# Optimization experiments

Hardware: AMD Instinct MI355X
Metric: run time of the kernel (lower is better)

## Reference

```python
import jax, jax.numpy as jnp
import numpy as np

# CUBA-LIF constants (from LavaNetwork.__init__ with beta=0.95)
THRESHOLD = 1.0
CURRENT_DECAY = 1.0   # current[t] = (1-1.0)*current[t-1] + input[t] == input[t]
VOLTAGE_DECAY = 1.0 - 0.95  # = 0.05, so v[t] = 0.95*v[t-1] + cur[t]

N_INPUT, N_HIDDEN, N_OUTPUT = 512, 2048, 4 * 64
B, T = 32, 1024


def setup_inputs() -> dict:
    key = jax.random.key(0)
    kx, k1, k2, k3, k4 = jax.random.split(key, 5)
    x = (jax.random.uniform(kx, (B, N_INPUT, T)) < 0.1).astype(jnp.float32)
    # learned params (Linear with bias); small scale so spiking is reasonable
    w1 = jax.random.normal(k1, (N_HIDDEN, N_INPUT), dtype=jnp.float32) * (1.0 / np.sqrt(N_INPUT))
    b1 = jax.random.normal(k2, (N_HIDDEN,), dtype=jnp.float32) * 0.01
    w2 = jax.random.normal(k3, (N_OUTPUT, N_HIDDEN), dtype=jnp.float32) * (1.0 / np.sqrt(N_HIDDEN))
    b2 = jax.random.normal(k4, (N_OUTPUT,), dtype=jnp.float32) * 0.01
    return {"x": x, "w1": w1, "b1": b1, "w2": w2, "b2": b2}


def _cuba_lif(cur):
    """CUBA neuron with current_decay=1 (current==synaptic input),
    leaky-integrate voltage, fire at threshold, reset voltage to 0.
    cur: (B, N, T) -> spikes (B, N, T)."""
    beta_v = 1.0 - VOLTAGE_DECAY  # 0.95

    def step(v, c_t):
        v = v * beta_v + c_t
        s = (v >= THRESHOLD).astype(v.dtype)
        v = v * (1.0 - s)  # reset-to-zero on spike (Loihi behavior)
        return v, s

    cur_t = jnp.moveaxis(cur, -1, 0)  # (T, B, N)
    v0 = jnp.zeros(cur.shape[:-1], cur.dtype)
    _, spk = jax.lax.scan(step, v0, cur_t)
    return jnp.moveaxis(spk, 0, -1)  # (B, N, T)


def reference(x, w1, b1, w2, b2):
    # layer 1: synapse (einsum 'bit,oi->bot' + bias) -> CUBA neuron
    cur1 = jnp.einsum('bit,oi->bot', x, w1) + b1[None, :, None]
    spk1 = _cuba_lif(cur1)
    # layer 2
    cur2 = jnp.einsum('bit,oi->bot', spk1, w2) + b2[None, :, None]
    spk2 = _cuba_lif(cur2)
    return (spk1, spk2)
```

## Files before the change

### kernel.cpp

```cpp
#include <hip/hip_runtime.h>


typedef int i32x4 __attribute__((ext_vector_type(4)));
typedef _Float16 f16x8 __attribute__((ext_vector_type(8)));
typedef _Float16 f16x4 __attribute__((ext_vector_type(4)));
typedef float f32x4 __attribute__((ext_vector_type(4)));

#define GLDS(g, l) __builtin_amdgcn_global_load_lds( \
    (const __attribute__((address_space(1))) void*)(g), \
    (__attribute__((address_space(3))) void*)(l), 16, 0, 0)

#define INV231 4.656612873077392578125e-10


__global__ __launch_bounds__(256) void prep_w8(const float* __restrict__ A,
                                               signed char* __restrict__ wp,
                                               int M, int K)
{
    long gt = (long)blockIdx.x * 256 + threadIdx.x;
    int kq4 = K >> 2;
    int m = (int)(gt / kq4), kq = (int)(gt % kq4);
    int k0 = kq * 4;
    int kt = k0 >> 6, kin = k0 & 63;
    int cw = ((kin >> 4) ^ (m >> 1)) & 3;
    float4 w = *(const float4*)&A[(long)m * K + k0];
    float wv[4] = {w.x, w.y, w.z, w.w};
    int pack[4] = {0, 0, 0, 0};
#pragma unroll
    for (int e = 0; e < 4; e++) {
        long k64 = (long)rint((double)wv[e] * 2147483648.0);
#pragma unroll
        for (int j = 0; j < 3; j++) {
            long r = ((k64 + 128) & 255) - 128;
            pack[j] |= ((int)r & 255) << (e * 8);
            k64 = (k64 - r) >> 8;
        }
        pack[3] |= ((int)k64 & 255) << (e * 8);
    }
#pragma unroll
    for (int p = 0; p < 4; p++)
        *(int*)&wp[(((long)kt * 4 + p) * M + m) * 64 + cw * 16 + (kin & 15)] = pack[p];
}

__global__ __launch_bounds__(256) void prep_x8(const float* __restrict__ x,
                                               unsigned char* __restrict__ xt)
{
    __shared__ float xs[64][68];
    const int b = blockIdx.z, i0 = blockIdx.y * 64, t0 = blockIdx.x * 64;
    const float* xb = x + ((long)b * 512 + i0) * 1024 + t0;
#pragma unroll
    for (int p = 0; p < 4; p++) {
        int f = threadIdx.x + p * 256;
        int i = f >> 4, t4 = (f & 15) * 4;
        *(float4*)&xs[i][t4] = *(const float4*)&xb[(long)i * 1024 + t4];
    }
    __syncthreads();
    int tt = threadIdx.x >> 2, c = threadIdx.x & 3;
    unsigned char bytes[16];
#pragma unroll
    for (int j = 0; j < 16; j++)
        bytes[j] = (unsigned char)xs[c * 16 + j][tt];
    *(uint4*)&xt[(((long)b * 8 + (i0 >> 6)) * 1024 + t0 + tt) * 64 + c * 16] =
        *(uint4*)bytes;
}

__global__ __launch_bounds__(320, 1) void gemm_lif1(
    const signed char* __restrict__ wp,
    const unsigned char* __restrict__ act,
    const float* __restrict__ bias,
    unsigned* __restrict__ mask_ws)
{
    __shared__ signed char Ws[8][4][64][64];
    __shared__ float cs[2][64][64];

    const int m0 = blockIdx.x * 64, b = blockIdx.y;
    const int tid = threadIdx.x, lane = tid & 63, wave = tid >> 6;
    const int lm = lane & 15, lq = lane >> 4;
    const int fro = ((lq ^ (lm >> 1)) & 3) * 16;
    const unsigned char* ab = act + (long)b * 8 * 1024 * 64;

    i32x4 areg[4][4];
    double bv = 0.0;

    if (wave < 4) {
        const int gl_row = lane >> 2, gl_col = (lane & 3) * 16;
#pragma unroll
        for (int j = 0; j < 8; ++j) {
            const int r = wave + 4 * j;
            const int kt = r >> 2, pl = r & 3;
            const signed char* g = wp + ((long)r * 2048 + m0 + gl_row) * 64 + gl_col;
#pragma unroll
            for (int q = 0; q < 4; ++q)
                GLDS(g + q * 16 * 64, &Ws[kt][pl][q * 16][0]);
        }
        bv = (double)bias[m0 + wave * 16 + lm];
#pragma unroll
        for (int f = 0; f < 4; f++)
            areg[0][f] = *(const i32x4*)
                &ab[((long)(f * 16 + lm)) * 64 + lq * 16];
#pragma unroll
        for (int f = 0; f < 4; f++)
            areg[1][f] = *(const i32x4*)
                &ab[((long)1 * 1024 + f * 16 + lm) * 64 + lq * 16];
    }
    __syncthreads();

    double u = 0.0;
    bool sprev = false;

    for (int p = 0; p < 17; ++p) {
        if (wave < 4 && p < 16) {
            i32x4 acc[4][4];
#pragma unroll
            for (int pp = 0; pp < 4; pp++)
#pragma unroll
                for (int f = 0; f < 4; f++) acc[pp][f] = (i32x4)0;

#pragma unroll
            for (int kk = 0; kk < 8; ++kk) {
                {
                    int vn = p * 8 + kk + 2;
                    if (vn > 127) vn = 127;
                    const int pn = vn >> 3, kn = vn & 7;
                    const long tt = (long)pn * 64 + lm;
#pragma unroll
                    for (int f = 0; f < 4; f++)
                        areg[(kk + 2) & 3][f] = *(const i32x4*)
                            &ab[((long)kn * 1024 + tt + f * 16) * 64 + lq * 16];
                }
                __builtin_amdgcn_s_setprio(1);
#pragma unroll
                for (int pl = 0; pl < 4; pl++) {
                    i32x4 w0 = *(const i32x4*)&Ws[kk][pl][wave * 16 + lm][fro];
#pragma unroll
                    for (int f = 0; f < 4; f++)
                        acc[pl][f] = __builtin_amdgcn_mfma_i32_16x16x64_i8(
                            areg[kk & 3][f], w0, acc[pl][f], 0, 0, 0);
                }
                __builtin_amdgcn_s_setprio(0);
            }
#pragma unroll
            for (int tf = 0; tf < 4; tf++)
#pragma unroll
                for (int r = 0; r < 4; r++) {
                    long T = acc[3][tf][r];
                    T = T * 256 + acc[2][tf][r];
                    T = T * 256 + acc[1][tf][r];
                    T = T * 256 + acc[0][tf][r];
                    cs[p & 1][tf * 16 + lq * 4 + r][wave * 16 + lm] =
                        (float)((double)T * INV231 + bv);
                }
        }
        if (wave == 4 && p >= 1) {
            const int pq = p - 1, buf = pq & 1;
            float cvA[32], cvB[32];
#pragma unroll
            for (int j = 0; j < 32; ++j) cvA[j] = cs[buf][j][lane];
#pragma unroll
            for (int j = 0; j < 32; ++j) cvB[j] = cs[buf][32 + j][lane];
            {
                unsigned mword = 0;
#pragma unroll
                for (int j = 0; j < 32; ++j) {
                    double c = (double)cvA[j];
                    double a = 0.95 * u + c;
                    u = sprev ? c : a;
                    bool s = (u >= 1.0);
                    mword |= (s ? 1u : 0u) << j;
                    sprev = s;
                }
                mask_ws[((long)b * 32 + pq * 2 + 0) * 2048 + m0 + lane] = mword;
            }
            {
                unsigned mword = 0;
#pragma unroll
                for (int j = 0; j < 32; ++j) {
                    double c = (double)cvB[j];
                    double a = 0.95 * u + c;
                    u = sprev ? c : a;
                    bool s = (u >= 1.0);
                    mword |= (s ? 1u : 0u) << j;
                    sprev = s;
                }
                mask_ws[((long)b * 32 + pq * 2 + 1) * 2048 + m0 + lane] = mword;
            }
        }
        asm volatile("s_waitcnt lgkmcnt(0)" ::: "memory");
        __builtin_amdgcn_s_barrier();
        __builtin_amdgcn_sched_barrier(0);
    }
}


__global__ __launch_bounds__(256) void expand_spk8(
    const unsigned* __restrict__ mask_ws,
    unsigned char* __restrict__ spk8)
{
    __shared__ unsigned msk[64][33];
    const int b = blockIdx.x, kt = blockIdx.y;
    const int tid = threadIdx.x;
#pragma unroll
    for (int i = 0; i < 8; ++i) {
        int idx = tid + i * 256;
        int tw = idx >> 6, m = idx & 63;
        msk[m][tw] = mask_ws[((long)b * 32 + tw) * 2048 + kt * 64 + m];
    }
    __syncthreads();
    unsigned char* dst = spk8 + ((long)b * 32 + kt) * 1024 * 64;
#pragma unroll
    for (int i = 0; i < 16; ++i) {
        int off = tid + i * 256;
        int t = off >> 2, mq = off & 3;
        int tw = t >> 5, sh = t & 31;
        unsigned w0 = 0, w1 = 0, w2 = 0, w3 = 0;
#pragma unroll
        for (int j = 0; j < 4; ++j) {
            w0 |= ((msk[mq * 16 + j][tw] >> sh) & 1u) << (8 * j);
            w1 |= ((msk[mq * 16 + 4 + j][tw] >> sh) & 1u) << (8 * j);
            w2 |= ((msk[mq * 16 + 8 + j][tw] >> sh) & 1u) << (8 * j);
            w3 |= ((msk[mq * 16 + 12 + j][tw] >> sh) & 1u) << (8 * j);
        }
        *(uint4*)&dst[(long)off * 16] = (uint4){w0, w1, w2, w3};
    }
}

__global__ __launch_bounds__(256) void expand_spk(
    const unsigned* __restrict__ mask_ws,
    float* __restrict__ spk1)
{
    __shared__ unsigned msk[8][32];
    const long rowbase = (long)blockIdx.x * 8;
    const int b = (int)(rowbase >> 11), m0 = (int)(rowbase & 2047);
    const int tid = threadIdx.x;
    {
        int w = tid >> 3, r = tid & 7;
        msk[r][w] = mask_ws[((long)b * 32 + w) * 2048 + m0 + r];
    }
    __syncthreads();
    const int r = tid >> 5, l5 = tid & 31;
    float* dst = spk1 + (rowbase + r) * 1024;
    const int sh = (l5 & 7) * 4;
#pragma unroll
    for (int j = 0; j < 8; j++) {
        const int t = l5 * 4 + j * 128;
        const unsigned w = msk[r][(l5 >> 3) + j * 4];
        float4 o;
        o.x = ((w >> sh) & 1u) ? 1.f : 0.f;
        o.y = ((w >> (sh + 1)) & 1u) ? 1.f : 0.f;
        o.z = ((w >> (sh + 2)) & 1u) ? 1.f : 0.f;
        o.w = ((w >> (sh + 3)) & 1u) ? 1.f : 0.f;
        *(float4*)&dst[t] = o;
    }
}

template <bool TRANS, int NITER, int CHUNK>
__global__ __launch_bounds__(256, 2) void gemm_i8(
    const signed char* __restrict__ wp,
    const unsigned char* __restrict__ act,
    const float* __restrict__ bias,
    float* __restrict__ C,
    int M)
{
    constexpr int NCHUNK = NITER / CHUNK;
    __shared__ signed char Ws[CHUNK][4][32][64];

    const int b = blockIdx.y;
    const int m0 = blockIdx.z * 32, t0 = blockIdx.x * 256;
    const int tid = threadIdx.x, lane = tid & 63, wave = tid >> 6;
    const int wt = t0 + wave * 64;
    const int lm = lane & 15, lq = lane >> 4;
    const int fro = ((lq ^ (lm >> 1)) & 3) * 16;
    const int gl_row = lane >> 2, gl_col = (lane & 3) * 16;

    const unsigned char* ab = act + (long)b * NITER * 1024 * 64;

    auto stage = [&](int cc) {
#pragma unroll
        for (int j = 0; j < CHUNK; ++j) {
            const int r = wave + 4 * j;
            const int kt = r >> 2, p = r & 3;
            const long kg = ((long)(cc * CHUNK + kt) * 4 + p);
            const signed char* g = wp + (kg * M + m0 + gl_row) * 64 + gl_col;
            GLDS(g, &Ws[kt][p][0][0]);
            GLDS(g + 16 * 64, &Ws[kt][p][16][0]);
        }
    };

    i32x4 acc[4][8];
#pragma unroll
    for (int p = 0; p < 4; p++)
#pragma unroll
        for (int q = 0; q < 8; q++) acc[p][q] = (i32x4)0;

    stage(0);
    i32x4 areg[2][4];
#pragma unroll
    for (int f = 0; f < 4; f++)
        areg[0][f] = *(const i32x4*)&ab[((long)(wt + f * 16 + lm)) * 64 + lq * 16];
    __syncthreads();

    for (int c = 0; c < NCHUNK; ++c) {
#pragma unroll
        for (int kk = 0; kk < CHUNK; ++kk) {
            {
                const int itv = c * CHUNK + kk;
                const long nx = (itv + 1 < NITER) ? itv + 1 : itv;
#pragma unroll
                for (int f = 0; f < 4; f++)
                    areg[(kk + 1) & 1][f] = *(const i32x4*)
                        &ab[(nx * 1024 + wt + f * 16 + lm) * 64 + lq * 16];
            }
#pragma unroll
            for (int p = 0; p < 4; p++) {
                i32x4 w0 = *(const i32x4*)&Ws[kk][p][lm][fro];
                i32x4 w1 = *(const i32x4*)&Ws[kk][p][16 + lm][fro];
                if (TRANS) {
#pragma unroll
                    for (int f = 0; f < 4; f++) {
                        acc[p][f * 2 + 0] = __builtin_amdgcn_mfma_i32_16x16x64_i8(
                            areg[kk & 1][f], w0, acc[p][f * 2 + 0], 0, 0, 0);
                        acc[p][f * 2 + 1] = __builtin_amdgcn_mfma_i32_16x16x64_i8(
                            areg[kk & 1][f], w1, acc[p][f * 2 + 1], 0, 0, 0);
                    }
                } else {
#pragma unroll
                    for (int f = 0; f < 4; f++) {
                        acc[p][0 + f] = __builtin_amdgcn_mfma_i32_16x16x64_i8(
                            w0, areg[kk & 1][f], acc[p][0 + f], 0, 0, 0);
                        acc[p][4 + f] = __builtin_amdgcn_mfma_i32_16x16x64_i8(
                            w1, areg[kk & 1][f], acc[p][4 + f], 0, 0, 0);
                    }
                }
            }
        }
        if (c + 1 < NCHUNK) {
            __syncthreads();
            stage(c + 1);
            __syncthreads();
        }
    }

    if (TRANS) {
        double bv[2];
        bv[0] = (double)bias[m0 + lm];
        bv[1] = (double)bias[m0 + 16 + lm];
        float* Cb = C + (long)b * 1024 * M;
#pragma unroll
        for (int tf = 0; tf < 4; tf++)
#pragma unroll
            for (int r = 0; r < 4; r++) {
                const int trow = wt + tf * 16 + lq * 4 + r;
#pragma unroll
                for (int mf = 0; mf < 2; mf++) {
                    long T = acc[3][tf * 2 + mf][r];
                    T = T * 256 + acc[2][tf * 2 + mf][r];
                    T = T * 256 + acc[1][tf * 2 + mf][r];
                    T = T * 256 + acc[0][tf * 2 + mf][r];
                    Cb[(long)trow * M + m0 + mf * 16 + lm] =
                        (float)((double)T * INV231 + bv[mf]);
                }
            }
    } else {
        float* Cb = C + (long)b * M * 1024;
#pragma unroll
        for (int mf = 0; mf < 2; mf++)
#pragma unroll
            for (int r = 0; r < 4; r++) {
                const int mrow = m0 + mf * 16 + lq * 4 + r;
                const double bv = (double)bias[mrow];
#pragma unroll
                for (int tf = 0; tf < 4; tf++) {
                    long T = acc[3][mf * 4 + tf][r];
                    T = T * 256 + acc[2][mf * 4 + tf][r];
                    T = T * 256 + acc[1][mf * 4 + tf][r];
                    T = T * 256 + acc[0][mf * 4 + tf][r];
                    Cb[(long)mrow * 1024 + wt + tf * 16 + lm] =
                        (float)((double)T * INV231 + bv);
                }
            }
    }
}

template <int RPB>
__global__ __launch_bounds__(256) void lif_lds(float* __restrict__ cur)
{
    __shared__ float cs[RPB][36];
    const long rowbase = (long)blockIdx.x * RPB;
    float* base = cur + rowbase * 1024;
    const int tid = threadIdx.x;
    double v = 0.0;
    const int NV = RPB * 32 / 4;
    for (int tc = 0; tc < 1024; tc += 32) {
        for (int f = tid; f < NV; f += 256) {
            int row = f >> 3, t4 = (f & 7) * 4;
            *(float4*)&cs[row][t4] = *(const float4*)&base[(long)row * 1024 + tc + t4];
        }
        __syncthreads();
        if (tid < RPB) {
            float cv[32];
#pragma unroll
            for (int j = 0; j < 32; j++) cv[j] = cs[tid][j];
#pragma unroll
            for (int j = 0; j < 32; j++) {
                v = 0.95 * v + (double)cv[j];
                bool s = v >= 1.0;
                cs[tid][j] = s ? 1.f : 0.f;
                if (s) v = 0.0;
            }
        }
        __syncthreads();
        for (int f = tid; f < NV; f += 256) {
            int row = f >> 3, t4 = (f & 7) * 4;
            *(float4*)&base[(long)row * 1024 + tc + t4] = *(float4*)&cs[row][t4];
        }
        __syncthreads();
    }
}


__device__ inline void split3(float w, _Float16& q0, _Float16& q1, _Float16& q2) {
    float p0 = rintf(w * 4096.f) * 2.44140625e-4f;
    float r1 = w - p0;
    float p1s = rintf(r1 * 8388608.f) * 2.44140625e-4f;
    float r2 = r1 - p1s * 4.8828125e-4f;
    float p2s = rintf(r2 * 1.7179869184e10f) * 1.220703125e-4f;
    q0 = (_Float16)p0; q1 = (_Float16)p1s; q2 = (_Float16)p2s;
}

__global__ __launch_bounds__(256) void gemm_f16x3_kernel(
    const float* __restrict__ A, const float* __restrict__ Bmat,
    const float* __restrict__ bias, float* __restrict__ C,
    int M, int N, int K, long sB, long sC)
{
    __shared__ _Float16 As[3][128][40];
    __shared__ _Float16 Bsh[128][40];
    const int batch = blockIdx.z;
    const float* Bp = Bmat + (long)batch * sB;
    float* Cp = C + (long)batch * sC;
    const int m0 = blockIdx.y * 128, n0 = blockIdx.x * 128;
    const int tid = threadIdx.x, lane = tid & 63, wave = tid >> 6;
    const int wrow = (wave >> 1) * 64, wcol = (wave & 1) * 64;
    const int lm = lane & 15, lq = lane >> 4;
    const int a_mo = tid >> 3, a_kc = (tid & 7) * 4;
    const int b_kq = tid >> 5, b_nq = tid & 31;

    f32x4 acc[3][4][4];
#pragma unroll
    for (int p = 0; p < 3; p++)
#pragma unroll
        for (int i = 0; i < 4; i++)
#pragma unroll
            for (int j = 0; j < 4; j++) acc[p][i][j] = (f32x4)0.f;

    for (int k0 = 0; k0 < K; k0 += 32) {
#pragma unroll
        for (int i = 0; i < 4; i++) {
            const int m = i * 32 + a_mo;
            float4 w = *(const float4*)&A[(long)(m0 + m) * K + k0 + a_kc];
            _Float16 a0[4], a1[4], a2[4];
            split3(w.x, a0[0], a1[0], a2[0]);
            split3(w.y, a0[1], a1[1], a2[1]);
            split3(w.z, a0[2], a1[2], a2[2]);
            split3(w.w, a0[3], a1[3], a2[3]);
            *(f16x4*)&As[0][m][a_kc] = (f16x4){a0[0], a0[1], a0[2], a0[3]};
            *(f16x4*)&As[1][m][a_kc] = (f16x4){a1[0], a1[1], a1[2], a1[3]};
            *(f16x4*)&As[2][m][a_kc] = (f16x4){a2[0], a2[1], a2[2], a2[3]};
        }
        {
            float4 r0 = *(const float4*)&Bp[(long)(k0 + b_kq * 4 + 0) * N + n0 + b_nq * 4];
            float4 r1 = *(const float4*)&Bp[(long)(k0 + b_kq * 4 + 1) * N + n0 + b_nq * 4];
            float4 r2 = *(const float4*)&Bp[(long)(k0 + b_kq * 4 + 2) * N + n0 + b_nq * 4];
            float4 r3 = *(const float4*)&Bp[(long)(k0 + b_kq * 4 + 3) * N + n0 + b_nq * 4];
            *(f16x4*)&Bsh[b_nq * 4 + 0][b_kq * 4] =
                (f16x4){(_Float16)r0.x, (_Float16)r1.x, (_Float16)r2.x, (_Float16)r3.x};
            *(f16x4*)&Bsh[b_nq * 4 + 1][b_kq * 4] =
                (f16x4){(_Float16)r0.y, (_Float16)r1.y, (_Float16)r2.y, (_Float16)r3.y};
            *(f16x4*)&Bsh[b_nq * 4 + 2][b_kq * 4] =
                (f16x4){(_Float16)r0.z, (_Float16)r1.z, (_Float16)r2.z, (_Float16)r3.z};
            *(f16x4*)&Bsh[b_nq * 4 + 3][b_kq * 4] =
                (f16x4){(_Float16)r0.w, (_Float16)r1.w, (_Float16)r2.w, (_Float16)r3.w};
        }
        __syncthreads();
        f16x8 bf[4];
#pragma unroll
        for (int j = 0; j < 4; j++)
            bf[j] = *(const f16x8*)&Bsh[wcol + j * 16 + lm][lq * 8];
#pragma unroll
        for (int p = 0; p < 3; p++) {
            f16x8 af[4];
#pragma unroll
            for (int i = 0; i < 4; i++)
                af[i] = *(const f16x8*)&As[p][wrow + i * 16 + lm][lq * 8];
#pragma unroll
            for (int i = 0; i < 4; i++)
#pragma unroll
                for (int j = 0; j < 4; j++)
                    acc[p][i][j] = __builtin_amdgcn_mfma_f32_16x16x32_f16(
                        af[i], bf[j], acc[p][i][j], 0, 0, 0);
        }
        __syncthreads();
    }
#pragma unroll
    for (int i = 0; i < 4; i++)
#pragma unroll
        for (int r = 0; r < 4; r++) {
            const int row = m0 + wrow + i * 16 + lq * 4 + r;
            const double bv = (double)bias[row];
#pragma unroll
            for (int j = 0; j < 4; j++) {
                double s = (double)acc[0][i][j][r]
                         + (double)acc[1][i][j][r] * 4.8828125e-4
                         + (double)acc[2][i][j][r] * 4.76837158203125e-7 + bv;
                Cp[(long)row * N + n0 + wcol + j * 16 + lm] = (float)s;
            }
        }
}

__global__ __launch_bounds__(256) void lif_rows(float* __restrict__ data,
                                                long nrows, int T)
{
    long r = (long)blockIdx.x * blockDim.x + threadIdx.x;
    if (r >= nrows) return;
    float* p = data + r * (long)T;
    double v = 0.0;
    for (int t = 0; t < T; t += 4) {
        float4 c = *(float4*)(p + t);
        float4 s;
        v = 0.95 * v + (double)c.x; s.x = (v >= 1.0) ? 1.f : 0.f; if (v >= 1.0) v = 0.0;
        v = 0.95 * v + (double)c.y; s.y = (v >= 1.0) ? 1.f : 0.f; if (v >= 1.0) v = 0.0;
        v = 0.95 * v + (double)c.z; s.z = (v >= 1.0) ? 1.f : 0.f; if (v >= 1.0) v = 0.0;
        v = 0.95 * v + (double)c.w; s.w = (v >= 1.0) ? 1.f : 0.f; if (v >= 1.0) v = 0.0;
        *(float4*)(p + t) = s;
    }
}


extern "C" void kernel_launch(void* const* d_in, const int* in_sizes, int n_in,
                              void* d_out, int out_size, void* d_ws, size_t ws_size,
                              hipStream_t stream)
{
    const float* x  = (const float*)d_in[0];
    const float* w1 = (const float*)d_in[1];
    const float* b1 = (const float*)d_in[2];
    const float* w2 = (const float*)d_in[3];
    const float* b2 = (const float*)d_in[4];

    float* out  = (float*)d_out;
    float* spk1 = out;
    float* spk2 = out + (long)32 * 2048 * 1024;

    const size_t WP1 = 4194304;
    const size_t WP2 = 2097152;
    const size_t X8T = 16777216;
    const size_t SPK = 67108864;
    const size_t MSK = 8388608;
    const size_t NEED = WP1 + WP2 + X8T + SPK + MSK;

    if (ws_size >= NEED) {
        char* ws = (char*)d_ws;
        signed char* wp1 = (signed char*)ws;
        signed char* wp2 = (signed char*)(ws + WP1);
        unsigned char* x8t = (unsigned char*)(ws + WP1 + WP2);
        unsigned char* spk8 = (unsigned char*)(ws + WP1 + WP2 + X8T);
        unsigned* mask_ws = (unsigned*)(ws + WP1 + WP2 + X8T + SPK);

        prep_w8<<<1024, 256, 0, stream>>>(w1, wp1, 2048, 512);
        prep_w8<<<512, 256, 0, stream>>>(w2, wp2, 256, 2048);
        prep_x8<<<dim3(16, 8, 32), 256, 0, stream>>>(x, x8t);

        gemm_lif1<<<dim3(32, 32), 320, 0, stream>>>(wp1, x8t, b1, mask_ws);
        expand_spk8<<<dim3(32, 32), 256, 0, stream>>>(mask_ws, spk8);

        gemm_i8<false, 32, 8><<<dim3(4, 32, 8), 256, 0, stream>>>(
            wp2, spk8, b2, spk2, 256);
        lif_lds<32><<<256, 256, 0, stream>>>(spk2);

        expand_spk<<<8192, 256, 0, stream>>>(mask_ws, spk1);
    } else {
        gemm_f16x3_kernel<<<dim3(8, 16, 32), 256, 0, stream>>>(
            w1, x, b1, spk1, 2048, 1024, 512, (long)512 * 1024, (long)2048 * 1024);
        lif_rows<<<(65536 + 255) / 256, 256, 0, stream>>>(spk1, 65536, 1024);
        gemm_f16x3_kernel<<<dim3(8, 2, 32), 256, 0, stream>>>(
            w2, spk1, b2, spk2, 256, 1024, 2048, (long)2048 * 1024, (long)256 * 1024);
        lif_rows<<<(8192 + 255) / 256, 256, 0, stream>>>(spk2, 8192, 1024);
    }
}
```

Before: 623.7 us.

## Fuse spike expansion into layer-1 GEMM+LIF kernel and prefetch LDS weights

The LIF wave in gemm_lif1 now writes the int8 spike tensor and the float spk1 output directly, which removes the mask workspace and the two expand kernels. The float output is produced with wave shuffles that transpose the bitmasks, so each store is coalesced. The MFMA loop also double-buffers its LDS weight fragments in registers, loading them two steps ahead. The cost is that the single LIF wave per block now issues all of spk1's 256MB of stores, plus byte-wise strided spk8 stores. That could make this one wave the serial bottleneck of the pipeline.

```diff
diff --git a/kernel.cpp b/kernel.cpp
--- a/kernel.cpp
+++ b/kernel.cpp
@@ -68,7 +68,8 @@
     const signed char* __restrict__ wp,
     const unsigned char* __restrict__ act,
     const float* __restrict__ bias,
-    unsigned* __restrict__ mask_ws)
+    unsigned char* __restrict__ spk8,
+    float* __restrict__ spk1)
 {
     __shared__ signed char Ws[8][4][64][64];
     __shared__ float cs[2][64][64];
@@ -79,6 +80,9 @@
     const int fro = ((lq ^ (lm >> 1)) & 3) * 16;
     const unsigned char* ab = act + (long)b * 8 * 1024 * 64;
 
+    unsigned char* sp8 = spk8 + (((long)b * 32 + (m0 >> 6)) * 1024) * 64 + lane;
+    float* sp1 = spk1 + ((long)b * 2048 + m0) * 1024;
+
     i32x4 areg[4][4];
     double bv = 0.0;
 
@@ -115,6 +119,10 @@
             for (int pp = 0; pp < 4; pp++)
 #pragma unroll
                 for (int f = 0; f < 4; f++) acc[pp][f] = (i32x4)0;
+
+            i32x4 wreg[4];
+            wreg[0] = *(const i32x4*)&Ws[0][0][wave * 16 + lm][fro];
+            wreg[1] = *(const i32x4*)&Ws[0][1][wave * 16 + lm][fro];
 
 #pragma unroll
             for (int kk = 0; kk < 8; ++kk) {
@@ -131,11 +139,15 @@
                 __builtin_amdgcn_s_setprio(1);
 #pragma unroll
                 for (int pl = 0; pl < 4; pl++) {
-                    i32x4 w0 = *(const i32x4*)&Ws[kk][pl][wave * 16 + lm][fro];
+                    const int q = kk * 4 + pl;
+                    const int qn = q + 2;
+                    if (qn < 32)
+                        wreg[qn & 3] = *(const i32x4*)
+                            &Ws[qn >> 2][qn & 3][wave * 16 + lm][fro];
 #pragma unroll
                     for (int f = 0; f < 4; f++)
                         acc[pl][f] = __builtin_amdgcn_mfma_i32_16x16x64_i8(
-                            areg[kk & 3][f], w0, acc[pl][f], 0, 0, 0);
+                            areg[kk & 3][f], wreg[q & 3], acc[pl][f], 0, 0, 0);
                 }
                 __builtin_amdgcn_s_setprio(0);
             }
@@ -158,98 +170,40 @@
             for (int j = 0; j < 32; ++j) cvA[j] = cs[buf][j][lane];
 #pragma unroll
             for (int j = 0; j < 32; ++j) cvB[j] = cs[buf][32 + j][lane];
-            {
-                unsigned mword = 0;
-#pragma unroll
-                for (int j = 0; j < 32; ++j) {
-                    double c = (double)cvA[j];
-                    double a = 0.95 * u + c;
-                    u = sprev ? c : a;
-                    bool s = (u >= 1.0);
-                    mword |= (s ? 1u : 0u) << j;
-                    sprev = s;
-                }
-                mask_ws[((long)b * 32 + pq * 2 + 0) * 2048 + m0 + lane] = mword;
-            }
-            {
-                unsigned mword = 0;
-#pragma unroll
-                for (int j = 0; j < 32; ++j) {
-                    double c = (double)cvB[j];
-                    double a = 0.95 * u + c;
-                    u = sprev ? c : a;
-                    bool s = (u >= 1.0);
-                    mword |= (s ? 1u : 0u) << j;
-                    sprev = s;
-                }
-                mask_ws[((long)b * 32 + pq * 2 + 1) * 2048 + m0 + lane] = mword;
+            unsigned mwordA = 0, mwordB = 0;
+#pragma unroll
+            for (int j = 0; j < 32; ++j) {
+                double c = (double)cvA[j];
+                double a = 0.95 * u + c;
+                u = sprev ? c : a;
+                bool s = (u >= 1.0);
+                mwordA |= (s ? 1u : 0u) << j;
+                sprev = s;
+                sp8[(long)(pq * 64 + j) * 64] = s ? 1 : 0;
+            }
+#pragma unroll
+            for (int j = 0; j < 32; ++j) {
+                double c = (double)cvB[j];
+                double a = 0.95 * u + c;
+                u = sprev ? c : a;
+                bool s = (u >= 1.0);
+                mwordB |= (s ? 1u : 0u) << j;
+                sprev = s;
+                sp8[(long)(pq * 64 + 32 + j) * 64] = s ? 1 : 0;
+            }
+            float* sp1t = sp1 + pq * 64 + lane;
+#pragma unroll 4
+            for (int mm = 0; mm < 64; ++mm) {
+                unsigned wa = (unsigned)__shfl((int)mwordA, mm);
+                unsigned wb = (unsigned)__shfl((int)mwordB, mm);
+                unsigned sel = (lane < 32) ? wa : wb;
+                sp1t[(long)mm * 1024] =
+                    ((sel >> (lane & 31)) & 1u) ? 1.f : 0.f;
             }
         }
         asm volatile("s_waitcnt lgkmcnt(0)" ::: "memory");
         __builtin_amdgcn_s_barrier();
         __builtin_amdgcn_sched_barrier(0);
-    }
-}
-
-
-__global__ __launch_bounds__(256) void expand_spk8(
-    const unsigned* __restrict__ mask_ws,
-    unsigned char* __restrict__ spk8)
-{
-    __shared__ unsigned msk[64][33];
-    const int b = blockIdx.x, kt = blockIdx.y;
-    const int tid = threadIdx.x;
-#pragma unroll
-    for (int i = 0; i < 8; ++i) {
-        int idx = tid + i * 256;
-        int tw = idx >> 6, m = idx & 63;
-        msk[m][tw] = mask_ws[((long)b * 32 + tw) * 2048 + kt * 64 + m];
-    }
-    __syncthreads();
-    unsigned char* dst = spk8 + ((long)b * 32 + kt) * 1024 * 64;
-#pragma unroll
-    for (int i = 0; i < 16; ++i) {
-        int off = tid + i * 256;
-        int t = off >> 2, mq = off & 3;
-        int tw = t >> 5, sh = t & 31;
-        unsigned w0 = 0, w1 = 0, w2 = 0, w3 = 0;
-#pragma unroll
-        for (int j = 0; j < 4; ++j) {
-            w0 |= ((msk[mq * 16 + j][tw] >> sh) & 1u) << (8 * j);
-            w1 |= ((msk[mq * 16 + 4 + j][tw] >> sh) & 1u) << (8 * j);
-            w2 |= ((msk[mq * 16 + 8 + j][tw] >> sh) & 1u) << (8 * j);
-            w3 |= ((msk[mq * 16 + 12 + j][tw] >> sh) & 1u) << (8 * j);
-        }
-        *(uint4*)&dst[(long)off * 16] = (uint4){w0, w1, w2, w3};
-    }
-}
-
-__global__ __launch_bounds__(256) void expand_spk(
-    const unsigned* __restrict__ mask_ws,
-    float* __restrict__ spk1)
-{
-    __shared__ unsigned msk[8][32];
-    const long rowbase = (long)blockIdx.x * 8;
-    const int b = (int)(rowbase >> 11), m0 = (int)(rowbase & 2047);
-    const int tid = threadIdx.x;
-    {
-        int w = tid >> 3, r = tid & 7;
-        msk[r][w] = mask_ws[((long)b * 32 + w) * 2048 + m0 + r];
-    }
-    __syncthreads();
-    const int r = tid >> 5, l5 = tid & 31;
-    float* dst = spk1 + (rowbase + r) * 1024;
-    const int sh = (l5 & 7) * 4;
-#pragma unroll
-    for (int j = 0; j < 8; j++) {
-        const int t = l5 * 4 + j * 128;
-        const unsigned w = msk[r][(l5 >> 3) + j * 4];
-        float4 o;
-        o.x = ((w >> sh) & 1u) ? 1.f : 0.f;
-        o.y = ((w >> (sh + 1)) & 1u) ? 1.f : 0.f;
-        o.z = ((w >> (sh + 2)) & 1u) ? 1.f : 0.f;
-        o.w = ((w >> (sh + 3)) & 1u) ? 1.f : 0.f;
-        *(float4*)&dst[t] = o;
     }
 }
 
@@ -553,8 +507,7 @@
     const size_t WP2 = 2097152;
     const size_t X8T = 16777216;
     const size_t SPK = 67108864;
-    const size_t MSK = 8388608;
-    const size_t NEED = WP1 + WP2 + X8T + SPK + MSK;
+    const size_t NEED = WP1 + WP2 + X8T + SPK;
 
     if (ws_size >= NEED) {
         char* ws = (char*)d_ws;
@@ -562,20 +515,16 @@
         signed char* wp2 = (signed char*)(ws + WP1);
         unsigned char* x8t = (unsigned char*)(ws + WP1 + WP2);
         unsigned char* spk8 = (unsigned char*)(ws + WP1 + WP2 + X8T);
-        unsigned* mask_ws = (unsigned*)(ws + WP1 + WP2 + X8T + SPK);
 
         prep_w8<<<1024, 256, 0, stream>>>(w1, wp1, 2048, 512);
         prep_w8<<<512, 256, 0, stream>>>(w2, wp2, 256, 2048);
         prep_x8<<<dim3(16, 8, 32), 256, 0, stream>>>(x, x8t);
 
-        gemm_lif1<<<dim3(32, 32), 320, 0, stream>>>(wp1, x8t, b1, mask_ws);
-        expand_spk8<<<dim3(32, 32), 256, 0, stream>>>(mask_ws, spk8);
+        gemm_lif1<<<dim3(32, 32), 320, 0, stream>>>(wp1, x8t, b1, spk8, spk1);
 
         gemm_i8<false, 32, 8><<<dim3(4, 32, 8), 256, 0, stream>>>(
             wp2, spk8, b2, spk2, 256);
         lif_lds<32><<<256, 256, 0, stream>>>(spk2);
-
-        expand_spk<<<8192, 256, 0, stream>>>(mask_ws, spk1);
     } else {
         gemm_f16x3_kernel<<<dim3(8, 16, 32), 256, 0, stream>>>(
             w1, x, b1, spk1, 2048, 1024, 512, (long)512 * 1024, (long)2048 * 1024);
```

After: 749.3 us. 20.1% more time.
